# Kernel tuning notes

Measured on AMD Instinct MI355X. Metric: run time of the kernel, lower is better.

Reference implementation:

```python
import jax, jax.numpy as jnp
import numpy as np

N_NODES = 100000
N_EDGES = 1600000
IN_F = 67
H1, C1 = 10, 8   # heads, per-head channels layer 1
H2, C2 = 1, 1    # layer 2


def setup_inputs() -> dict:
    key = jax.random.key(0)
    ks = jax.random.split(key, 10)
    x = jax.random.normal(ks[0], (N_NODES, IN_F), dtype=jnp.float32)
    edge_index = jax.random.randint(ks[1], (2, N_EDGES), 0, N_NODES, dtype=jnp.int64)
    s = 0.1
    W1 = jax.random.normal(ks[2], (IN_F, H1 * C1), dtype=jnp.float32) * s
    att_src1 = jax.random.normal(ks[3], (H1, C1), dtype=jnp.float32) * s
    att_dst1 = jax.random.normal(ks[4], (H1, C1), dtype=jnp.float32) * s
    b1 = jnp.zeros((H1 * C1,), dtype=jnp.float32)
    W2 = jax.random.normal(ks[5], (H1 * C1, H2 * C2), dtype=jnp.float32) * s
    att_src2 = jax.random.normal(ks[6], (H2, C2), dtype=jnp.float32) * s
    att_dst2 = jax.random.normal(ks[7], (H2, C2), dtype=jnp.float32) * s
    b2 = jnp.zeros((H2 * C2,), dtype=jnp.float32)
    return {"x": x, "edge_index": edge_index, "W1": W1, "att_src1": att_src1,
            "att_dst1": att_dst1, "b1": b1, "W2": W2, "att_src2": att_src2,
            "att_dst2": att_dst2, "b2": b2}


def gat_conv(x, src, dst, W, att_src, att_dst, bias, heads, out_ch):
    """PyG GATConv (eval mode): gather -> leaky_relu -> segment softmax -> scatter."""
    n = x.shape[0]
    h = (x @ W).reshape(n, heads, out_ch)                     # [N,H,C]
    a_src = jnp.sum(h * att_src, axis=-1)                     # [N,H]
    a_dst = jnp.sum(h * att_dst, axis=-1)                     # [N,H]
    e = a_src[src] + a_dst[dst]                               # [E,H]
    e = jax.nn.leaky_relu(e, negative_slope=0.2)
    # numerically stable softmax over edges grouped by destination node
    m = jax.ops.segment_max(e, dst, num_segments=n)           # [N,H]
    ex = jnp.exp(e - m[dst])
    denom = jax.ops.segment_sum(ex, dst, num_segments=n)      # [N,H]
    alpha = ex / denom[dst]                                   # [E,H]
    msg = h[src] * alpha[:, :, None]                          # [E,H,C]
    out = jax.ops.segment_sum(msg, dst, num_segments=n)       # [N,H,C]
    return out.reshape(n, heads * out_ch) + bias


def reference(x, edge_index, W1, att_src1, att_dst1, b1, W2, att_src2, att_dst2, b2):
    n = x.shape[0]
    loops = jnp.arange(n, dtype=edge_index.dtype)
    src = jnp.concatenate([edge_index[0], loops])             # add_self_loops=True
    dst = jnp.concatenate([edge_index[1], loops])
    h = gat_conv(x, src, dst, W1, att_src1, att_dst1, b1, H1, C1)
    h = jax.nn.elu(h)
    out = gat_conv(h, src, dst, W2, att_src2, att_dst2, b2, H2, C2)
    return out
```

## Files before the change

### kernel.cpp

```cpp
#include <hip/hip_runtime.h>
#include <math.h>

#define IN_F 67
#define F1   80
#define NH1  10
#define NC1  8

#define GN   64
#define KS   104
#define PKS  96

#define RB    128
#define RSH   7
#define NGRP  8
#define BCAP  512
#define SLCAP 3072
#define CSTRIDE 16
#define NFILLB 512

typedef _Float16 h16;
typedef h16 h16x2 __attribute__((ext_vector_type(2)));
typedef h16 h16x8 __attribute__((ext_vector_type(8)));
typedef float f32x4 __attribute__((ext_vector_type(4)));
typedef float f32x4u __attribute__((ext_vector_type(4), aligned(4)));
typedef int i32x4 __attribute__((ext_vector_type(4)));

__global__ __launch_bounds__(256)
void k_front(const float* __restrict__ x, const float* __restrict__ W,
             const float* __restrict__ att_s, const float* __restrict__ att_d,
             const int* __restrict__ ei, int* __restrict__ bcur,
             int2* __restrict__ ebuf, h16* __restrict__ pk,
             float* __restrict__ a_dst, int N, int E, int NB) {
    __shared__ __align__(16) char smem[GN * 81 * 4];
    h16*   sWt = (h16*)smem;
    float* sO  = (float*)smem;

    const int tid = threadIdx.x;

    if ((int)blockIdx.x < NFILLB) {
        int g = blockIdx.x & (NGRP - 1);
        const int E4 = E & ~3;
        int stride4 = NFILLB * 256 * 4;
        for (int e = (blockIdx.x * 256 + tid) * 4; e < E4; e += stride4) {
            i32x4 sv = *(const i32x4*)(ei + e);
            i32x4 dv = *(const i32x4*)(ei + E + e);
#pragma unroll
            for (int j = 0; j < 4; ++j) {
                int d = dv[j];
                int b = d >> RSH;
                size_t slot = (size_t)(g * NB + b);
                int p = atomicAdd(&bcur[slot * CSTRIDE], 1);
                if (p < BCAP) ebuf[slot * BCAP + p] = make_int2(sv[j], d);
            }
        }
        for (int e = E4 + blockIdx.x * 256 + tid; e < E; e += NFILLB * 256) {
            int s = ei[e], d = ei[E + e];
            int b = d >> RSH;
            size_t slot = (size_t)(g * NB + b);
            int p = atomicAdd(&bcur[slot * CSTRIDE], 1);
            if (p < BCAP) ebuf[slot * BCAP + p] = make_int2(s, d);
        }
        return;
    }

    const int node0 = (blockIdx.x - NFILLB) * GN;

    if (tid < 240) {
        int c = tid - (tid >= 160 ? 160 : (tid >= 80 ? 80 : 0));
        int kb = (tid >= 160 ? 64 : (tid >= 80 ? 32 : 0));
        h16 tmp[32];
#pragma unroll
        for (int j = 0; j < 32; ++j) {
            int k = kb + j;
            tmp[j] = (h16)((k < IN_F) ? W[k * F1 + c] : 0.f);
        }
        h16* dst = sWt + c * KS + kb;
#pragma unroll
        for (int j = 0; j < 4; ++j)
            *(h16x8*)(dst + j * 8) = *(const h16x8*)(tmp + j * 8);
    }
    __syncthreads();

    const int lane = tid & 63;
    const int m    = lane & 15;
    const int quad = lane >> 4;
    const int wn0  = (tid >> 6) * 16;

    int gn  = node0 + wn0 + m;
    int gnc = gn < N ? gn : N - 1;
    const float* xr = x + (size_t)gnc * IN_F;

    f32x4 acc[5];
#pragma unroll
    for (int ct = 0; ct < 5; ++ct) acc[ct] = (f32x4){0.f, 0.f, 0.f, 0.f};

#pragma unroll
    for (int ks = 0; ks < 64; ks += 32) {
        int k0 = ks + quad * 8;
        f32x4 a0 = *(const f32x4u*)(xr + k0);
        f32x4 a1 = *(const f32x4u*)(xr + k0 + 4);
        h16x8 af;
        af[0] = (h16)a0.x; af[1] = (h16)a0.y; af[2] = (h16)a0.z; af[3] = (h16)a0.w;
        af[4] = (h16)a1.x; af[5] = (h16)a1.y; af[6] = (h16)a1.z; af[7] = (h16)a1.w;
#pragma unroll
        for (int ct = 0; ct < 5; ++ct) {
            h16x8 bf = *(const h16x8*)(sWt + (ct * 16 + m) * KS + ks + quad * 8);
            acc[ct] = __builtin_amdgcn_mfma_f32_16x16x32_f16(af, bf, acc[ct], 0, 0, 0);
        }
    }
    {
        h16x8 af = (h16x8)(h16)0.f;
        if (quad == 0) {
            af[0] = (h16)xr[64]; af[1] = (h16)xr[65]; af[2] = (h16)xr[66];
        }
#pragma unroll
        for (int ct = 0; ct < 5; ++ct) {
            h16x8 bf = *(const h16x8*)(sWt + (ct * 16 + m) * KS + 64 + quad * 8);
            acc[ct] = __builtin_amdgcn_mfma_f32_16x16x32_f16(af, bf, acc[ct], 0, 0, 0);
        }
    }
    __syncthreads();

#pragma unroll
    for (int ct = 0; ct < 5; ++ct)
#pragma unroll
        for (int r = 0; r < 4; ++r)
            sO[(wn0 + quad * 4 + r) * 81 + ct * 16 + m] = acc[ct][r];
    __syncthreads();

    for (int idx = tid; idx < GN * (F1 / 2); idx += 256) {
        int n = idx / (F1 / 2);
        int p = idx - n * (F1 / 2);
        int g = node0 + n;
        if (g < N) {
            h16x2 v;
            v.x = (h16)sO[n * 81 + 2 * p];
            v.y = (h16)sO[n * 81 + 2 * p + 1];
            *(h16x2*)(pk + (size_t)g * PKS + 2 * p) = v;
        }
    }
    for (int t = tid; t < GN * NH1; t += 256) {
        int n = t / NH1;
        int h = t - n * NH1;
        int g = node0 + n;
        if (g < N) {
            const float* hr = sO + n * 81 + h * NC1;
            float s = 0.f, d = 0.f;
#pragma unroll
            for (int c = 0; c < NC1; ++c) {
                float v = hr[c];
                s += v * att_s[h * NC1 + c];
                d += v * att_d[h * NC1 + c];
            }
            pk[(size_t)g * PKS + F1 + h] = (h16)s;
            a_dst[g * NH1 + h] = d;
        }
    }
}

__global__ __launch_bounds__(256)
void k_agg1(const int2* __restrict__ ebuf, const int* __restrict__ bcur,
            const h16* __restrict__ pk, const float* __restrict__ a_dst,
            const float* __restrict__ b1, const float* __restrict__ W2,
            const float* __restrict__ att_s2, const float* __restrict__ att_d2,
            float2* __restrict__ hs2, float* __restrict__ a_dst2,
            int* __restrict__ row, int* __restrict__ deg, int* __restrict__ csr2,
            int N, int NB) {
    __shared__ int   s_cnt[RB];
    __shared__ int   s_scan[RB];
    __shared__ int   s_cur[RB];
    __shared__ float s_acc[RB];
    __shared__ int   sList[SLCAP];

    const int tid = threadIdx.x;
    const int b = blockIdx.x;
    const int lo = b * RB;

    for (int i = tid; i < RB; i += 256) { s_cnt[i] = 1; s_acc[i] = 0.f; }
    __syncthreads();

    for (int g = 0; g < NGRP; ++g) {
        size_t slot = (size_t)(g * NB + b);
        int cnt = bcur[slot * CSTRIDE];
        cnt = cnt < BCAP ? cnt : BCAP;
        const int2* eb = ebuf + slot * BCAP;
        for (int i = tid; i < cnt; i += 256)
            atomicAdd(&s_cnt[eb[i].y - lo], 1);
    }
    __syncthreads();

    if (tid < RB) s_scan[tid] = s_cnt[tid];
    __syncthreads();
    for (int o = 1; o < RB; o <<= 1) {
        int v = 0;
        if (tid < RB && tid >= o) v = s_scan[tid - o];
        __syncthreads();
        if (tid < RB) s_scan[tid] += v;
        __syncthreads();
    }
    if (tid < RB) {
        int excl = s_scan[tid] - s_cnt[tid];
        int n = lo + tid;
        if (excl < SLCAP) sList[excl] = n;
        s_cur[tid] = excl + 1;
        if (n < N) {
            int dg = s_cnt[tid];
            if (excl + dg > SLCAP) dg = SLCAP - excl > 0 ? SLCAP - excl : 0;
            row[n] = b * SLCAP + excl;
            deg[n] = dg;
        }
    }
    __syncthreads();

    for (int g = 0; g < NGRP; ++g) {
        size_t slot = (size_t)(g * NB + b);
        int cnt = bcur[slot * CSTRIDE];
        cnt = cnt < BCAP ? cnt : BCAP;
        const int2* eb = ebuf + slot * BCAP;
        for (int i = tid; i < cnt; i += 256) {
            int2 e = eb[i];
            int p = atomicAdd(&s_cur[e.y - lo], 1);
            if (p < SLCAP) sList[p] = e.x;
        }
    }
    __syncthreads();

    int total = s_scan[RB - 1];
    total = total < SLCAP ? total : SLCAP;
    for (int i = tid; i < total; i += 256)
        csr2[(size_t)b * SLCAP + i] = sList[i];

    for (int t = tid; t < RB * NH1; t += 256) {
        int n_l = t / NH1;
        int h = t - n_l * NH1;
        int n = lo + n_l;
        if (n >= N) continue;
        int beg = s_scan[n_l] - s_cnt[n_l];
        int end = beg + s_cnt[n_l];
        end = end < SLCAP ? end : SLCAP;
        float ad = a_dst[n * NH1 + h];
        float den = 0.f;
        float num[NC1];
#pragma unroll
        for (int c = 0; c < NC1; ++c) num[c] = 0.f;

        int i = beg;
        for (; i + 3 < end; i += 4) {
            int sv[4];
#pragma unroll
            for (int j = 0; j < 4; ++j) sv[j] = sList[i + j];
            h16x8 q[4];
            float a[4];
#pragma unroll
            for (int j = 0; j < 4; ++j) {
                const h16* rp = pk + (size_t)sv[j] * PKS;
                q[j] = *(const h16x8*)(rp + h * NC1);
                a[j] = (float)rp[F1 + h];
            }
#pragma unroll
            for (int j = 0; j < 4; ++j) {
                float v = a[j] + ad;
                v = v > 0.f ? v : 0.2f * v;
                float w = __expf(v);
                den += w;
#pragma unroll
                for (int c = 0; c < NC1; ++c) num[c] += w * (float)q[j][c];
            }
        }
        for (; i < end; ++i) {
            const h16* rp = pk + (size_t)sList[i] * PKS;
            h16x8 q = *(const h16x8*)(rp + h * NC1);
            float v = (float)rp[F1 + h] + ad;
            v = v > 0.f ? v : 0.2f * v;
            float w = __expf(v);
            den += w;
#pragma unroll
            for (int c = 0; c < NC1; ++c) num[c] += w * (float)q[c];
        }
        float inv = 1.f / den;
        const float* bb = b1 + h * NC1;
        const float* w2 = W2 + h * NC1;
        float p = 0.f;
#pragma unroll
        for (int c = 0; c < NC1; ++c) {
            float o = num[c] * inv + bb[c];
            o = o > 0.f ? o : expm1f(o);
            p += o * w2[c];
        }
        atomicAdd(&s_acc[n_l], p);
    }
    __syncthreads();

    if (tid < RB) {
        int n = lo + tid;
        if (n < N) {
            float acc = s_acc[tid];
            float2 v;
            v.x = acc;
            v.y = acc * att_s2[0];
            hs2[n] = v;
            a_dst2[n] = acc * att_d2[0];
        }
    }
}

__global__ __launch_bounds__(256)
void k_agg2(const int* __restrict__ row, const int* __restrict__ deg,
            const int* __restrict__ csr2, const float2* __restrict__ hs2,
            const float* __restrict__ a_dst2, const float* __restrict__ b2,
            float* __restrict__ out, int N) {
    int n = blockIdx.x * blockDim.x + threadIdx.x;
    if (n >= N) return;
    float ad = a_dst2[n];
    float den = 0.f, num = 0.f;
    int beg = row[n];
    int end = beg + deg[n];
    int i = beg;
    for (; i + 7 < end; i += 8) {
        int sv[8];
#pragma unroll
        for (int j = 0; j < 8; ++j) sv[j] = csr2[i + j];
        float2 g[8];
#pragma unroll
        for (int j = 0; j < 8; ++j) g[j] = hs2[sv[j]];
#pragma unroll
        for (int j = 0; j < 8; ++j) {
            float v = g[j].y + ad;
            v = v > 0.f ? v : 0.2f * v;
            float w = __expf(v);
            den += w;
            num += w * g[j].x;
        }
    }
    for (; i < end; ++i) {
        float2 g = hs2[csr2[i]];
        float v = g.y + ad;
        v = v > 0.f ? v : 0.2f * v;
        float w = __expf(v);
        den += w;
        num += w * g.x;
    }
    out[n] = num / den + b2[0];
}

extern "C" void kernel_launch(void* const* d_in, const int* in_sizes, int n_in,
                              void* d_out, int out_size, void* d_ws, size_t ws_size,
                              hipStream_t stream) {
    const float* x        = (const float*)d_in[0];
    const int*   ei       = (const int*)d_in[1];
    const float* W1       = (const float*)d_in[2];
    const float* att_src1 = (const float*)d_in[3];
    const float* att_dst1 = (const float*)d_in[4];
    const float* b1       = (const float*)d_in[5];
    const float* W2       = (const float*)d_in[6];
    const float* att_src2 = (const float*)d_in[7];
    const float* att_dst2 = (const float*)d_in[8];
    const float* b2       = (const float*)d_in[9];
    float* out = (float*)d_out;

    const int N  = in_sizes[0] / IN_F;
    const int E  = in_sizes[1] / 2;
    const int NB = (N + RB - 1) / RB;

    float*  ws      = (float*)d_ws;
    h16*    pk      = (h16*)ws;
    float*  a_dst1  = ws + (size_t)N * (PKS / 2);
    float2* hs2     = (float2*)(a_dst1 + (size_t)N * NH1);
    float*  a_dst2  = (float*)(hs2 + N);
    int*    row     = (int*)(a_dst2 + N);
    int*    deg     = row + N;
    int*    bcur    = deg + N;
    int*    csr2    = bcur + (size_t)NGRP * NB * CSTRIDE;
    int2*   ebuf    = (int2*)(csr2 + (size_t)NB * SLCAP);

    const int B = 256;
    const int nbG = (N + GN - 1) / GN;

    hipMemsetAsync(bcur, 0, (size_t)NGRP * NB * CSTRIDE * sizeof(int), stream);
    k_front<<<NFILLB + nbG, 256, 0, stream>>>(x, W1, att_src1, att_dst1, ei,
                                              bcur, ebuf, pk, a_dst1, N, E, NB);

    k_agg1<<<NB, 256, 0, stream>>>(ebuf, bcur, pk, a_dst1, b1, W2,
                                   att_src2, att_dst2, hs2, a_dst2,
                                   row, deg, csr2, N, NB);

    k_agg2<<<(N + B - 1) / B, B, 0, stream>>>(row, deg, csr2, hs2, a_dst2, b2, out, N);
}
```

Baseline: 257.0 us.

## Bin edges per block in shared memory before global coarse-bucket scatter

The edge-bucketing pass now stages each 2048-edge chunk in shared memory, counts and scans per coarse 512-node bucket, and reserves global slots with one atomic per bucket instead of one global atomic per edge. Edges are packed into a single int (17-bit source plus local destination), which halves buffer traffic. k_agg1 reads a coarse bucket shared by four blocks, keeps only its own quarter in a shared temp list, and builds the CSR from shared memory, so it no longer scans global memory twice. Each block must now read four times more bucket data and filter it. Packing source indices into 17 bits assumes N stays below 131072.

```diff
diff --git a/kernel.cpp b/kernel.cpp
--- a/kernel.cpp
+++ b/kernel.cpp
@@ -10,13 +10,16 @@
 #define KS   104
 #define PKS  96
 
+#define CB    512
+#define CSH   9
+#define NBC   196
 #define RB    128
-#define RSH   7
 #define NGRP  8
-#define BCAP  512
+#define GCAP  1536
 #define SLCAP 3072
 #define CSTRIDE 16
-#define NFILLB 512
+#define NFB   512
+#define CHUNK 2048
 
 typedef _Float16 h16;
 typedef h16 h16x2 __attribute__((ext_vector_type(2)));
@@ -28,42 +31,79 @@
 __global__ __launch_bounds__(256)
 void k_front(const float* __restrict__ x, const float* __restrict__ W,
              const float* __restrict__ att_s, const float* __restrict__ att_d,
-             const int* __restrict__ ei, int* __restrict__ bcur,
-             int2* __restrict__ ebuf, h16* __restrict__ pk,
-             float* __restrict__ a_dst, int N, int E, int NB) {
+             const int* __restrict__ ei, int* __restrict__ gcur,
+             int* __restrict__ ebuf, h16* __restrict__ pk,
+             float* __restrict__ a_dst, int N, int E) {
     __shared__ __align__(16) char smem[GN * 81 * 4];
+    const int tid = threadIdx.x;
+
+    if ((int)blockIdx.x < NFB) {
+        int2* sStage = (int2*)smem;
+        int*  sCnt   = (int*)(smem + CHUNK * 8);
+        int*  sGBase = sCnt + NBC;
+        int*  sScan  = sGBase + NBC;
+        const int g = blockIdx.x & (NGRP - 1);
+
+        for (int base_e = blockIdx.x * CHUNK; base_e < E; base_e += NFB * CHUNK) {
+            int lim = E - base_e; if (lim > CHUNK) lim = CHUNK;
+            for (int i = tid; i < NBC; i += 256) sCnt[i] = 0;
+            __syncthreads();
+
+            int2 ev[8]; int pos[8]; int nloc = 0;
+            int e0 = base_e + tid * 8;
+            if (tid * 8 + 8 <= lim) {
+                i32x4 s0 = *(const i32x4*)(ei + e0);
+                i32x4 s1 = *(const i32x4*)(ei + e0 + 4);
+                i32x4 d0 = *(const i32x4*)(ei + E + e0);
+                i32x4 d1 = *(const i32x4*)(ei + E + e0 + 4);
+#pragma unroll
+                for (int j = 0; j < 4; ++j) { ev[j] = make_int2(s0[j], d0[j]); }
+#pragma unroll
+                for (int j = 0; j < 4; ++j) { ev[4 + j] = make_int2(s1[j], d1[j]); }
+                nloc = 8;
+            } else {
+                for (int j = 0; j < 8; ++j) {
+                    int e = e0 + j;
+                    if (tid * 8 + j < lim) { ev[nloc++] = make_int2(ei[e], ei[E + e]); }
+                }
+            }
+            for (int j = 0; j < nloc; ++j)
+                pos[j] = atomicAdd(&sCnt[ev[j].y >> CSH], 1);
+            __syncthreads();
+
+            int v = (tid < NBC) ? sCnt[tid] : 0;
+            sScan[tid] = v;
+            __syncthreads();
+            for (int o = 1; o < 256; o <<= 1) {
+                int u = (tid >= o) ? sScan[tid - o] : 0;
+                __syncthreads();
+                sScan[tid] += u;
+                __syncthreads();
+            }
+            for (int j = 0; j < nloc; ++j) {
+                int B = ev[j].y >> CSH;
+                sStage[sScan[B] - sCnt[B] + pos[j]] = ev[j];
+            }
+            if (tid < NBC && sCnt[tid] > 0)
+                sGBase[tid] = atomicAdd(&gcur[((size_t)g * NBC + tid) * CSTRIDE], sCnt[tid]);
+            __syncthreads();
+
+            int total = sScan[NBC - 1];
+            for (int i = tid; i < total; i += 256) {
+                int2 e = sStage[i];
+                int B = e.y >> CSH;
+                int gp = sGBase[B] + (i - (sScan[B] - sCnt[B]));
+                if (gp < GCAP)
+                    ebuf[((size_t)g * NBC + B) * GCAP + gp] = e.x | ((e.y & (CB - 1)) << 17);
+            }
+            __syncthreads();
+        }
+        return;
+    }
+
     h16*   sWt = (h16*)smem;
     float* sO  = (float*)smem;
-
-    const int tid = threadIdx.x;
-
-    if ((int)blockIdx.x < NFILLB) {
-        int g = blockIdx.x & (NGRP - 1);
-        const int E4 = E & ~3;
-        int stride4 = NFILLB * 256 * 4;
-        for (int e = (blockIdx.x * 256 + tid) * 4; e < E4; e += stride4) {
-            i32x4 sv = *(const i32x4*)(ei + e);
-            i32x4 dv = *(const i32x4*)(ei + E + e);
-#pragma unroll
-            for (int j = 0; j < 4; ++j) {
-                int d = dv[j];
-                int b = d >> RSH;
-                size_t slot = (size_t)(g * NB + b);
-                int p = atomicAdd(&bcur[slot * CSTRIDE], 1);
-                if (p < BCAP) ebuf[slot * BCAP + p] = make_int2(sv[j], d);
-            }
-        }
-        for (int e = E4 + blockIdx.x * 256 + tid; e < E; e += NFILLB * 256) {
-            int s = ei[e], d = ei[E + e];
-            int b = d >> RSH;
-            size_t slot = (size_t)(g * NB + b);
-            int p = atomicAdd(&bcur[slot * CSTRIDE], 1);
-            if (p < BCAP) ebuf[slot * BCAP + p] = make_int2(s, d);
-        }
-        return;
-    }
-
-    const int node0 = (blockIdx.x - NFILLB) * GN;
+    const int node0 = (blockIdx.x - NFB) * GN;
 
     if (tid < 240) {
         int c = tid - (tid >= 160 ? 160 : (tid >= 80 ? 80 : 0));
@@ -131,19 +171,19 @@
     for (int idx = tid; idx < GN * (F1 / 2); idx += 256) {
         int n = idx / (F1 / 2);
         int p = idx - n * (F1 / 2);
-        int g = node0 + n;
-        if (g < N) {
+        int gg = node0 + n;
+        if (gg < N) {
             h16x2 v;
             v.x = (h16)sO[n * 81 + 2 * p];
             v.y = (h16)sO[n * 81 + 2 * p + 1];
-            *(h16x2*)(pk + (size_t)g * PKS + 2 * p) = v;
+            *(h16x2*)(pk + (size_t)gg * PKS + 2 * p) = v;
         }
     }
     for (int t = tid; t < GN * NH1; t += 256) {
         int n = t / NH1;
         int h = t - n * NH1;
-        int g = node0 + n;
-        if (g < N) {
+        int gg = node0 + n;
+        if (gg < N) {
             const float* hr = sO + n * 81 + h * NC1;
             float s = 0.f, d = 0.f;
 #pragma unroll
@@ -152,40 +192,53 @@
                 s += v * att_s[h * NC1 + c];
                 d += v * att_d[h * NC1 + c];
             }
-            pk[(size_t)g * PKS + F1 + h] = (h16)s;
-            a_dst[g * NH1 + h] = d;
+            pk[(size_t)gg * PKS + F1 + h] = (h16)s;
+            a_dst[gg * NH1 + h] = d;
         }
     }
 }
 
 __global__ __launch_bounds__(256)
-void k_agg1(const int2* __restrict__ ebuf, const int* __restrict__ bcur,
+void k_agg1(const int* __restrict__ ebuf, const int* __restrict__ gcur,
             const h16* __restrict__ pk, const float* __restrict__ a_dst,
             const float* __restrict__ b1, const float* __restrict__ W2,
             const float* __restrict__ att_s2, const float* __restrict__ att_d2,
             float2* __restrict__ hs2, float* __restrict__ a_dst2,
             int* __restrict__ row, int* __restrict__ deg, int* __restrict__ csr2,
             int N, int NB) {
+    __shared__ int   sTmp[SLCAP];
+    __shared__ int   sList[SLCAP];
     __shared__ int   s_cnt[RB];
     __shared__ int   s_scan[RB];
     __shared__ int   s_cur[RB];
     __shared__ float s_acc[RB];
-    __shared__ int   sList[SLCAP];
+    __shared__ int   sTot;
 
     const int tid = threadIdx.x;
     const int b = blockIdx.x;
+    const int B = b >> 2;
+    const int q = b & 3;
     const int lo = b * RB;
 
     for (int i = tid; i < RB; i += 256) { s_cnt[i] = 1; s_acc[i] = 0.f; }
+    if (tid == 0) sTot = 0;
     __syncthreads();
 
     for (int g = 0; g < NGRP; ++g) {
-        size_t slot = (size_t)(g * NB + b);
-        int cnt = bcur[slot * CSTRIDE];
-        cnt = cnt < BCAP ? cnt : BCAP;
-        const int2* eb = ebuf + slot * BCAP;
-        for (int i = tid; i < cnt; i += 256)
-            atomicAdd(&s_cnt[eb[i].y - lo], 1);
+        size_t slot = (size_t)g * NBC + B;
+        int cnt = gcur[slot * CSTRIDE];
+        cnt = cnt < GCAP ? cnt : GCAP;
+        const int* eb = ebuf + slot * GCAP;
+        for (int i = tid; i < cnt; i += 256) {
+            int v = eb[i];
+            int dloc = v >> 17;
+            if ((dloc >> 7) == q) {
+                int n_l = dloc & (RB - 1);
+                atomicAdd(&s_cnt[n_l], 1);
+                int p = atomicAdd(&sTot, 1);
+                if (p < SLCAP) sTmp[p] = (v & 0x1FFFF) | (n_l << 17);
+            }
+        }
     }
     __syncthreads();
 
@@ -212,22 +265,18 @@
     }
     __syncthreads();
 
-    for (int g = 0; g < NGRP; ++g) {
-        size_t slot = (size_t)(g * NB + b);
-        int cnt = bcur[slot * CSTRIDE];
-        cnt = cnt < BCAP ? cnt : BCAP;
-        const int2* eb = ebuf + slot * BCAP;
-        for (int i = tid; i < cnt; i += 256) {
-            int2 e = eb[i];
-            int p = atomicAdd(&s_cur[e.y - lo], 1);
-            if (p < SLCAP) sList[p] = e.x;
-        }
-    }
-    __syncthreads();
-
-    int total = s_scan[RB - 1];
-    total = total < SLCAP ? total : SLCAP;
-    for (int i = tid; i < total; i += 256)
+    int total = sTot < SLCAP ? sTot : SLCAP;
+    for (int i = tid; i < total; i += 256) {
+        int u = sTmp[i];
+        int n_l = u >> 17;
+        int p = atomicAdd(&s_cur[n_l], 1);
+        if (p < SLCAP) sList[p] = u & 0x1FFFF;
+    }
+    __syncthreads();
+
+    int tot2 = s_scan[RB - 1];
+    tot2 = tot2 < SLCAP ? tot2 : SLCAP;
+    for (int i = tid; i < tot2; i += 256)
         csr2[(size_t)b * SLCAP + i] = sList[i];
 
     for (int t = tid; t < RB * NH1; t += 256) {
@@ -249,12 +298,12 @@
             int sv[4];
 #pragma unroll
             for (int j = 0; j < 4; ++j) sv[j] = sList[i + j];
-            h16x8 q[4];
+            h16x8 qf[4];
             float a[4];
 #pragma unroll
             for (int j = 0; j < 4; ++j) {
                 const h16* rp = pk + (size_t)sv[j] * PKS;
-                q[j] = *(const h16x8*)(rp + h * NC1);
+                qf[j] = *(const h16x8*)(rp + h * NC1);
                 a[j] = (float)rp[F1 + h];
             }
 #pragma unroll
@@ -264,18 +313,18 @@
                 float w = __expf(v);
                 den += w;
 #pragma unroll
-                for (int c = 0; c < NC1; ++c) num[c] += w * (float)q[j][c];
+                for (int c = 0; c < NC1; ++c) num[c] += w * (float)qf[j][c];
             }
         }
         for (; i < end; ++i) {
             const h16* rp = pk + (size_t)sList[i] * PKS;
-            h16x8 q = *(const h16x8*)(rp + h * NC1);
+            h16x8 qf = *(const h16x8*)(rp + h * NC1);
             float v = (float)rp[F1 + h] + ad;
             v = v > 0.f ? v : 0.2f * v;
             float w = __expf(v);
             den += w;
 #pragma unroll
-            for (int c = 0; c < NC1; ++c) num[c] += w * (float)q[c];
+            for (int c = 0; c < NC1; ++c) num[c] += w * (float)qf[c];
         }
         float inv = 1.f / den;
         const float* bb = b1 + h * NC1;
@@ -369,18 +418,18 @@
     float*  a_dst2  = (float*)(hs2 + N);
     int*    row     = (int*)(a_dst2 + N);
     int*    deg     = row + N;
-    int*    bcur    = deg + N;
-    int*    csr2    = bcur + (size_t)NGRP * NB * CSTRIDE;
-    int2*   ebuf    = (int2*)(csr2 + (size_t)NB * SLCAP);
+    int*    gcur    = deg + N;
+    int*    csr2    = gcur + (size_t)NGRP * NBC * CSTRIDE;
+    int*    ebuf    = csr2 + (size_t)NB * SLCAP;
 
     const int B = 256;
     const int nbG = (N + GN - 1) / GN;
 
-    hipMemsetAsync(bcur, 0, (size_t)NGRP * NB * CSTRIDE * sizeof(int), stream);
-    k_front<<<NFILLB + nbG, 256, 0, stream>>>(x, W1, att_src1, att_dst1, ei,
-                                              bcur, ebuf, pk, a_dst1, N, E, NB);
-
-    k_agg1<<<NB, 256, 0, stream>>>(ebuf, bcur, pk, a_dst1, b1, W2,
+    hipMemsetAsync(gcur, 0, (size_t)NGRP * NBC * CSTRIDE * sizeof(int), stream);
+    k_front<<<NFB + nbG, 256, 0, stream>>>(x, W1, att_src1, att_dst1, ei,
+                                           gcur, ebuf, pk, a_dst1, N, E);
+
+    k_agg1<<<NB, 256, 0, stream>>>(ebuf, gcur, pk, a_dst1, b1, W2,
                                    att_src2, att_dst2, hs2, a_dst2,
                                    row, deg, csr2, N, NB);
 
```

Measured after the change: 218.6 us. 1.18x faster.
